# Kernel tuning notes

Hardware: AMD Instinct MI355X
Metric: run time of the kernel (lower is better)

## Reference

```python
import jax, jax.numpy as jnp
import numpy as np

N = 500_000      # total rows (e.g. video frames)
S = 10_000       # number of segments (shots)
D_IN = 128
D_OUT = 128


def setup_inputs() -> dict:
    key = jax.random.key(0)
    k1, k2, k3 = jax.random.split(key, 3)
    inp = jax.random.normal(k1, (N, D_IN), dtype=jnp.float32)
    # contiguous non-overlapping segments covering [0, N): graph[j] = (start_j, end_j) inclusive
    rng = np.random.default_rng(0)
    cuts = np.sort(rng.choice(np.arange(1, N), size=S - 1, replace=False))
    starts = np.concatenate([[0], cuts]).astype(np.int64)
    ends = np.concatenate([cuts - 1, [N - 1]]).astype(np.int64)
    graph = jnp.asarray(np.stack([starts, ends], axis=1))  # [S, 2]
    # nn.Linear params (kaiming-uniform-ish scale is irrelevant for correctness baseline)
    W = jax.random.normal(k2, (D_OUT, D_IN), dtype=jnp.float32) * (1.0 / np.sqrt(D_IN))
    b = jax.random.normal(k3, (D_OUT,), dtype=jnp.float32) * 0.01
    return {"input": inp, "graph": graph, "W": W, "b": b}


def reference(input, graph, W, b):
    # One big GEMM for the projection (instead of per-segment Linear calls) ...
    y = input @ W.T + b                              # [N, D_OUT]
    n = input.shape[0]
    s = graph.shape[0]
    starts = graph[:, 0]
    ends = graph[:, 1]
    rows = jnp.arange(n)
    # ... then a single irregular segment reduction over ragged boundaries.
    seg_id = jnp.clip(jnp.searchsorted(starts, rows, side="right") - 1, 0, s - 1)  # [N]
    valid = (rows >= starts[seg_id]) & (rows <= ends[seg_id])  # guards any uncovered rows
    y = jnp.where(valid[:, None], y, 0.0)
    return jax.ops.segment_sum(y, seg_id, num_segments=s)     # [S, D_OUT]
```

## Files before the change

kernel.cpp:

```cpp
#include <hip/hip_runtime.h>
#include <hip/hip_bf16.h>


#define D 128
#define D4 32
#define WROWS 128

__device__ __forceinline__ void f4add(float4& a, const float4& v) {
  a.x += v.x; a.y += v.y; a.z += v.z; a.w += v.w;
}

__global__ __launch_bounds__(256) void zero_xs_kernel(float4* Xs4, int n4) {
  int i = blockIdx.x * 256 + threadIdx.x;
  if (i < n4) Xs4[i] = make_float4(0.f, 0.f, 0.f, 0.f);
}

__global__ __launch_bounds__(256) void seg_sum_wave_kernel(
    const float* __restrict__ in, const int* __restrict__ graph,
    float* __restrict__ Xs, int N, int S) {
  int lane = threadIdx.x & 63;
  int wv   = threadIdx.x >> 6;
  int win  = blockIdx.x * 4 + wv;
  int w0   = win * WROWS;
  if (w0 >= N) return;
  int wEnd = min(w0 + WROWS, N) - 1;

  int c4 = lane & 31;
  int rh = lane >> 5;

  int lo = 0, hi = S - 1;
  while (lo < hi) {
    int mid = (lo + hi + 1) >> 1;
    if (graph[2 * mid] <= w0) lo = mid; else hi = mid - 1;
  }

  const float4* in4 = (const float4*)in;
  int s = lo;
  while (true) {
    int rs       = graph[2 * s];
    int reRaw    = graph[2 * s + 1];
    int nxtStart = (s + 1 < S) ? graph[2 * s + 2] : N;
    int re       = min(reRaw, min(nxtStart - 1, N - 1));
    int rs_c     = max(rs, 0);
    int a        = max(rs_c, w0);
    int b2       = min(re, wEnd);

    if (a <= b2) {
      int len = b2 - a + 1;
      const float4* p = in4 + (size_t)(a + rh) * D4 + c4;
      float4 A0 = make_float4(0.f,0.f,0.f,0.f);
      float4 A1 = make_float4(0.f,0.f,0.f,0.f);
      float4 A2 = make_float4(0.f,0.f,0.f,0.f);
      float4 A3 = make_float4(0.f,0.f,0.f,0.f);
      int r = 0;
      for (; r + 8 <= len; r += 8) {
        float4 v0 = p[(size_t)(r + 0) * D4];
        float4 v1 = p[(size_t)(r + 2) * D4];
        float4 v2 = p[(size_t)(r + 4) * D4];
        float4 v3 = p[(size_t)(r + 6) * D4];
        f4add(A0, v0); f4add(A1, v1); f4add(A2, v2); f4add(A3, v3);
      }
      for (; r + rh < len; r += 2)
        f4add(A0, p[(size_t)r * D4]);
      f4add(A0, A1); f4add(A2, A3); f4add(A0, A2);

      float4 o;
      o.x = __shfl_xor(A0.x, 32, 64);
      o.y = __shfl_xor(A0.y, 32, 64);
      o.z = __shfl_xor(A0.z, 32, 64);
      o.w = __shfl_xor(A0.w, 32, 64);
      f4add(A0, o);

      bool full = (rs_c >= w0) && (re <= wEnd);
      if (lane < 32) {
        if (full) {
          ((float4*)Xs)[(size_t)s * D4 + c4] = A0;
        } else {
          float* q = Xs + (size_t)s * D + c4 * 4;
          atomicAdd(q + 0, A0.x);
          atomicAdd(q + 1, A0.y);
          atomicAdd(q + 2, A0.z);
          atomicAdd(q + 3, A0.w);
        }
      }
    }
    if (s + 1 >= S || graph[2 * s + 2] > wEnd) break;
    ++s;
  }
}

#define SEG_PB 16
#define OUT_PB 64
#define WT_STRIDE 65

__global__ __launch_bounds__(256) void seg_gemm_kernel(
    const float* __restrict__ Xs, const float* __restrict__ W,
    const float* __restrict__ b, const int* __restrict__ graph,
    float* __restrict__ out, int N, int S) {
  __shared__ float Wt[D * WT_STRIDE];
  __shared__ __align__(16) float XsL[SEG_PB * D];
  __shared__ float cntL[SEG_PB];

  int tid   = threadIdx.x;
  int s0    = blockIdx.x * SEG_PB;
  int oBase = blockIdx.y * OUT_PB;

  #pragma unroll
  for (int rnd = 0; rnd < 8; ++rnd) {
    int linear = rnd * 256 + tid;
    int op     = linear >> 5;
    int d4     = (linear & 31) << 2;
    float4 w = *(const float4*)(W + (oBase + op) * D + d4);
    Wt[(d4 + 0) * WT_STRIDE + op] = w.x;
    Wt[(d4 + 1) * WT_STRIDE + op] = w.y;
    Wt[(d4 + 2) * WT_STRIDE + op] = w.z;
    Wt[(d4 + 3) * WT_STRIDE + op] = w.w;
  }
  {
    const float4* src = (const float4*)(Xs + s0 * D);
    float4* dst = (float4*)XsL;
    dst[tid]       = src[tid];
    dst[tid + 256] = src[tid + 256];
  }
  if (tid < SEG_PB) {
    int s   = s0 + tid;
    int rs  = graph[2 * s];
    int re  = graph[2 * s + 1];
    int nxt = (s + 1 < S) ? (graph[2 * s + 2] - 1) : (N - 1);
    re = min(re, min(nxt, N - 1));
    rs = max(rs, 0);
    cntL[tid] = (float)max(0, re - rs + 1);
  }
  __syncthreads();

  int op = tid & 63;
  int g  = tid >> 6;
  float acc[4] = {0.f, 0.f, 0.f, 0.f};

  const float4* xs4 = (const float4*)XsL;
  #pragma unroll 8
  for (int d4 = 0; d4 < D4; ++d4) {
    float w0 = Wt[(4 * d4 + 0) * WT_STRIDE + op];
    float w1 = Wt[(4 * d4 + 1) * WT_STRIDE + op];
    float w2 = Wt[(4 * d4 + 2) * WT_STRIDE + op];
    float w3 = Wt[(4 * d4 + 3) * WT_STRIDE + op];
    #pragma unroll
    for (int j = 0; j < 4; ++j) {
      float4 x = xs4[(4 * j + g) * D4 + d4];
      acc[j] += x.x * w0 + x.y * w1 + x.z * w2 + x.w * w3;
    }
  }

  float bo = b[oBase + op];
  #pragma unroll
  for (int j = 0; j < 4; ++j) {
    int sl = 4 * j + g;
    out[(s0 + sl) * D + oBase + op] = acc[j] + cntL[sl] * bo;
  }
}

extern "C" void kernel_launch(void* const* d_in, const int* in_sizes, int n_in,
                              void* d_out, int out_size, void* d_ws, size_t ws_size,
                              hipStream_t stream) {
  const float* in    = (const float*)d_in[0];
  const int*   graph = (const int*)d_in[1];
  const float* W     = (const float*)d_in[2];
  const float* b     = (const float*)d_in[3];
  float* out = (float*)d_out;

  const int N = in_sizes[0] / D;
  const int S = in_sizes[1] / 2;

  float* Xs = (float*)d_ws;

  int n4 = S * D4;
  zero_xs_kernel<<<(n4 + 255) / 256, 256, 0, stream>>>((float4*)Xs, n4);

  int nWaves  = (N + WROWS - 1) / WROWS;
  int nBlocks = (nWaves + 3) / 4;
  seg_sum_wave_kernel<<<nBlocks, 256, 0, stream>>>(in, graph, Xs, N, S);

  dim3 grid2(S / SEG_PB, D / OUT_PB);
  seg_gemm_kernel<<<grid2, 256, 0, stream>>>(Xs, W, b, graph, out, N, S);
}
```

Measured before the change: 381.5 us.

## Replace atomic partial sums with per-window buffer merged in GEMM kernel

The segment-sum kernel no longer uses atomicAdd for segments that span window boundaries. The owning window writes the segment head directly, and every other window writes its partial into a per-window buffer. The GEMM kernel adds those partials back when it loads Xs, which removes both the atomics and the separate zeroing kernel launch. The main load loop is also unrolled to 16 rows. This adds a serial merge loop in the GEMM prologue and relies on each window holding at most one continuing-segment partial.

```diff
diff --git a/kernel.cpp b/kernel.cpp
--- a/kernel.cpp
+++ b/kernel.cpp
@@ -10,14 +10,9 @@
   a.x += v.x; a.y += v.y; a.z += v.z; a.w += v.w;
 }
 
-__global__ __launch_bounds__(256) void zero_xs_kernel(float4* Xs4, int n4) {
-  int i = blockIdx.x * 256 + threadIdx.x;
-  if (i < n4) Xs4[i] = make_float4(0.f, 0.f, 0.f, 0.f);
-}
-
 __global__ __launch_bounds__(256) void seg_sum_wave_kernel(
     const float* __restrict__ in, const int* __restrict__ graph,
-    float* __restrict__ Xs, int N, int S) {
+    float* __restrict__ Xs, float* __restrict__ Bb, int N, int S) {
   int lane = threadIdx.x & 63;
   int wv   = threadIdx.x >> 6;
   int win  = blockIdx.x * 4 + wv;
@@ -53,12 +48,25 @@
       float4 A2 = make_float4(0.f,0.f,0.f,0.f);
       float4 A3 = make_float4(0.f,0.f,0.f,0.f);
       int r = 0;
-      for (; r + 8 <= len; r += 8) {
+      for (; r + 16 <= len; r += 16) {
+        float4 v0 = p[(size_t)(r +  0) * D4];
+        float4 v1 = p[(size_t)(r +  2) * D4];
+        float4 v2 = p[(size_t)(r +  4) * D4];
+        float4 v3 = p[(size_t)(r +  6) * D4];
+        float4 v4 = p[(size_t)(r +  8) * D4];
+        float4 v5 = p[(size_t)(r + 10) * D4];
+        float4 v6 = p[(size_t)(r + 12) * D4];
+        float4 v7 = p[(size_t)(r + 14) * D4];
+        f4add(A0, v0); f4add(A1, v1); f4add(A2, v2); f4add(A3, v3);
+        f4add(A0, v4); f4add(A1, v5); f4add(A2, v6); f4add(A3, v7);
+      }
+      if (r + 8 <= len) {
         float4 v0 = p[(size_t)(r + 0) * D4];
         float4 v1 = p[(size_t)(r + 2) * D4];
         float4 v2 = p[(size_t)(r + 4) * D4];
         float4 v3 = p[(size_t)(r + 6) * D4];
         f4add(A0, v0); f4add(A1, v1); f4add(A2, v2); f4add(A3, v3);
+        r += 8;
       }
       for (; r + rh < len; r += 2)
         f4add(A0, p[(size_t)r * D4]);
@@ -71,16 +79,11 @@
       o.w = __shfl_xor(A0.w, 32, 64);
       f4add(A0, o);
 
-      bool full = (rs_c >= w0) && (re <= wEnd);
       if (lane < 32) {
-        if (full) {
+        if (rs_c >= w0) {
           ((float4*)Xs)[(size_t)s * D4 + c4] = A0;
         } else {
-          float* q = Xs + (size_t)s * D + c4 * 4;
-          atomicAdd(q + 0, A0.x);
-          atomicAdd(q + 1, A0.y);
-          atomicAdd(q + 2, A0.z);
-          atomicAdd(q + 3, A0.w);
+          ((float4*)Bb)[(size_t)win * D4 + c4] = A0;
         }
       }
     }
@@ -94,9 +97,9 @@
 #define WT_STRIDE 65
 
 __global__ __launch_bounds__(256) void seg_gemm_kernel(
-    const float* __restrict__ Xs, const float* __restrict__ W,
-    const float* __restrict__ b, const int* __restrict__ graph,
-    float* __restrict__ out, int N, int S) {
+    const float* __restrict__ Xs, const float* __restrict__ Bb,
+    const float* __restrict__ W, const float* __restrict__ b,
+    const int* __restrict__ graph, float* __restrict__ out, int N, int S) {
   __shared__ float Wt[D * WT_STRIDE];
   __shared__ __align__(16) float XsL[SEG_PB * D];
   __shared__ float cntL[SEG_PB];
@@ -130,6 +133,33 @@
     re = min(re, min(nxt, N - 1));
     rs = max(rs, 0);
     cntL[tid] = (float)max(0, re - rs + 1);
+  }
+  __syncthreads();
+
+  {
+    int seg  = tid >> 4;
+    int part = tid & 15;
+    int s    = s0 + seg;
+    int rs   = max(graph[2 * s], 0);
+    int nxt  = (s + 1 < S) ? graph[2 * s + 2] : N;
+    int re   = min(graph[2 * s + 1], min(nxt - 1, N - 1));
+    float4* x4 = (float4*)XsL + seg * D4 + part * 2;
+    if (re < rs) {
+      x4[0] = make_float4(0.f,0.f,0.f,0.f);
+      x4[1] = make_float4(0.f,0.f,0.f,0.f);
+    } else {
+      int wOwn  = rs >> 7;
+      int wLast = re >> 7;
+      if (wLast > wOwn) {
+        float4 x0 = x4[0], x1 = x4[1];
+        const float4* bb4 = (const float4*)Bb;
+        for (int w = wOwn + 1; w <= wLast; ++w) {
+          f4add(x0, bb4[(size_t)w * D4 + part * 2]);
+          f4add(x1, bb4[(size_t)w * D4 + part * 2 + 1]);
+        }
+        x4[0] = x0; x4[1] = x1;
+      }
+    }
   }
   __syncthreads();
 
@@ -171,15 +201,13 @@
   const int N = in_sizes[0] / D;
   const int S = in_sizes[1] / 2;
 
+  int nWaves  = (N + WROWS - 1) / WROWS;
   float* Xs = (float*)d_ws;
-
-  int n4 = S * D4;
-  zero_xs_kernel<<<(n4 + 255) / 256, 256, 0, stream>>>((float4*)Xs, n4);
-
-  int nWaves  = (N + WROWS - 1) / WROWS;
+  float* Bb = Xs + (size_t)S * D;
+
   int nBlocks = (nWaves + 3) / 4;
-  seg_sum_wave_kernel<<<nBlocks, 256, 0, stream>>>(in, graph, Xs, N, S);
+  seg_sum_wave_kernel<<<nBlocks, 256, 0, stream>>>(in, graph, Xs, Bb, N, S);
 
   dim3 grid2(S / SEG_PB, D / OUT_PB);
-  seg_gemm_kernel<<<grid2, 256, 0, stream>>>(Xs, W, b, graph, out, N, S);
-}
+  seg_gemm_kernel<<<grid2, 256, 0, stream>>>(Xs, Bb, W, b, graph, out, N, S);
+}
```

New measurement: 382.3 us. About the same (+0.2%).
